# Performance work log

Measured on AMD Instinct MI355X. Metric: run time of the kernel, lower is better.

The kernel has to match this reference:

```python
import jax, jax.numpy as jnp
import numpy as np

D_MODEL = 1024
D_STATE = 128
HEAD_DIM = 64
EXPAND = 2
K = 4  # conv_kernel
N_GROUPS = 1
D_INNER = EXPAND * D_MODEL            # 2048
N_HEADS = D_INNER // HEAD_DIM         # 32
D_PROJ = 2 * D_INNER + 2 * N_GROUPS * D_STATE + N_HEADS  # 4384
EPS = 1e-6


def _rmsnorm(x, w):
    return x * jax.lax.rsqrt(jnp.mean(x * x, axis=-1, keepdims=True) + EPS) * w


def setup_inputs() -> dict:
    key = jax.random.key(0)
    ks = jax.random.split(key, 8)
    B, L = 2, 2048
    x = jax.random.normal(ks[0], (B, L, D_MODEL), jnp.float32)
    norm_w = jnp.ones((D_MODEL,), jnp.float32)
    in_proj_w = jax.random.normal(ks[1], (D_PROJ, D_MODEL), jnp.float32) / np.sqrt(D_MODEL).astype(np.float32)
    conv_w = jax.random.normal(ks[2], (D_INNER, K), jnp.float32) / np.sqrt(K).astype(np.float32)
    conv_b = jnp.zeros((D_INNER,), jnp.float32)
    A_log = jnp.log(jax.random.uniform(ks[3], (N_HEADS,), jnp.float32) * 15.0 + 1.0)
    D = jnp.ones((N_HEADS,), jnp.float32)
    dt_bias = jnp.log(jax.random.uniform(ks[4], (N_HEADS,), jnp.float32) * 0.099 + 0.001)
    out_proj_w = jax.random.normal(ks[5], (D_MODEL, D_INNER), jnp.float32) / np.sqrt(D_INNER).astype(np.float32)
    return dict(x=x, norm_w=norm_w, in_proj_w=in_proj_w, conv_w=conv_w, conv_b=conv_b,
                A_log=A_log, D=D, dt_bias=dt_bias, out_proj_w=out_proj_w)


def reference(x, norm_w, in_proj_w, conv_w, conv_b, A_log, D, dt_bias, out_proj_w):
    batch, L, _ = x.shape
    residual = x
    xn = _rmsnorm(x, norm_w)
    proj = jnp.einsum('bld,pd->blp', xn, in_proj_w)  # (B,L,D_PROJ)

    # split fused projection -> z, x_ssm, B, C, dt_raw
    i = 0
    z = proj[:, :, i:i + D_INNER]; i += D_INNER
    x_ssm = proj[:, :, i:i + D_INNER]; i += D_INNER
    bc = N_GROUPS * D_STATE
    Bm = proj[:, :, i:i + bc].reshape(batch, L, N_GROUPS, D_STATE); i += bc
    Cm = proj[:, :, i:i + bc].reshape(batch, L, N_GROUPS, D_STATE); i += bc
    dt_raw = proj[:, :, i:i + N_HEADS]

    # causal depthwise conv1d (left-pad K-1) + SiLU
    xp = jnp.pad(x_ssm, ((0, 0), (K - 1, 0), (0, 0)))
    x_conv = conv_b
    for k in range(K):
        x_conv = x_conv + xp[:, k:k + L, :] * conv_w[:, k]
    x_conv = jax.nn.silu(x_conv)

    xh = x_conv.reshape(batch, L, N_HEADS, HEAD_DIM)
    dt = jax.nn.softplus(dt_raw + dt_bias)          # (B,L,H)
    dA = jnp.exp(-jnp.exp(A_log) * dt)              # (B,L,H)
    dtx = dt[..., None] * xh                        # (B,L,H,P)

    gidx = jnp.arange(N_HEADS) // (N_HEADS // N_GROUPS)
    Bg = Bm[:, :, gidx, :]                          # (B,L,H,N)
    Cg = Cm[:, :, gidx, :]                          # (B,L,H,N)

    def step(h, inp):
        dA_t, dtx_t, B_t, C_t = inp                 # (B,H), (B,H,P), (B,H,N), (B,H,N)
        h = h * dA_t[:, :, None, None] + dtx_t[..., None] * B_t[:, :, None, :]
        y_t = jnp.einsum('bhpn,bhn->bhp', h, C_t)
        return h, y_t

    h0 = jnp.zeros((batch, N_HEADS, HEAD_DIM, D_STATE), jnp.float32)
    xs = (jnp.swapaxes(dA, 0, 1), jnp.swapaxes(dtx, 0, 1),
          jnp.swapaxes(Bg, 0, 1), jnp.swapaxes(Cg, 0, 1))
    _, ys = jax.lax.scan(step, h0, xs)              # ys: (L,B,H,P)
    y = jnp.swapaxes(ys, 0, 1) + D[None, None, :, None] * xh

    y = y.reshape(batch, L, D_INNER) * jax.nn.silu(z)
    return residual + jnp.einsum('bli,di->bld', y, out_proj_w)
```

## Files before the change

### kernel.cpp

```cpp
#include <hip/hip_runtime.h>
#include <hip/hip_bf16.h>

#define L_SEQ 2048
#define DM 1024
#define DI 2048
#define DS 128
#define NH 32
#define HD 64
#define DPROJ 4384
#define DPAD 4480
#define NBATCH 2
#define NCH 8
#define CH 256
#define B_OFF 4096
#define C_OFF 4224
#define DT_OFF 4352
#define SWZ(row) ((((row) ^ ((row) >> 3)) & 7) << 4)

typedef unsigned short u16;
typedef __attribute__((ext_vector_type(8))) short short8;
typedef __attribute__((ext_vector_type(4))) float f32x4;

#define GLL16(g, l)                                                     \
  __builtin_amdgcn_global_load_lds(                                     \
      (const __attribute__((address_space(1))) unsigned int*)(g),       \
      (__attribute__((address_space(3))) unsigned int*)(l), 16, 0, 0)
#define VMCNT0 asm volatile("s_waitcnt vmcnt(0)" ::: "memory")
#define SBAR __builtin_amdgcn_s_barrier()
#define SGB0 __builtin_amdgcn_sched_barrier(0)

__device__ __forceinline__ u16 f2bf(float f) {
  union { float f; unsigned u; } c; c.f = f;
  unsigned u = c.u;
  u += 0x7fffu + ((u >> 16) & 1u);
  return (u16)(u >> 16);
}
__device__ __forceinline__ float bf2f(u16 u) {
  return __uint_as_float((unsigned)u << 16);
}
__device__ __forceinline__ float siluf(float x) {
  return x / (1.0f + expf(-x));
}
__device__ __forceinline__ void store_out(u16* C, size_t o, float v) { C[o] = f2bf(v); }
__device__ __forceinline__ void store_out(float* C, size_t o, float v) { C[o] = v; }

__global__ __launch_bounds__(256) void rmsnorm_kernel(
    const float* __restrict__ x, const float* __restrict__ w,
    u16* __restrict__ xnb) {
  int m = blockIdx.x;
  int t = threadIdx.x;
  const float* row = x + (size_t)m * DM;
  float4 v = *(const float4*)(row + t * 4);
  float ss = v.x * v.x + v.y * v.y + v.z * v.z + v.w * v.w;
#pragma unroll
  for (int o = 32; o > 0; o >>= 1) ss += __shfl_xor(ss, o);
  __shared__ float sred[4];
  if ((t & 63) == 0) sred[t >> 6] = ss;
  __syncthreads();
  ss = sred[0] + sred[1] + sred[2] + sred[3];
  float rs = rsqrtf(ss * (1.0f / DM) + 1e-6f);
  float4 wv = *(const float4*)(w + t * 4);
  ushort4 o;
  o.x = f2bf(v.x * rs * wv.x);
  o.y = f2bf(v.y * rs * wv.y);
  o.z = f2bf(v.z * rs * wv.z);
  o.w = f2bf(v.w * rs * wv.w);
  *(ushort4*)(xnb + (size_t)m * DM + t * 4) = o;
}

__global__ __launch_bounds__(256) void cvt_w1_kernel(
    const float* __restrict__ w, u16* __restrict__ o) {
  int r = blockIdx.x;
  int c = threadIdx.x * 4;
  ushort4 u;
  if (r < DPROJ) {
    float4 v = *(const float4*)(w + (size_t)r * DM + c);
    u.x = f2bf(v.x); u.y = f2bf(v.y); u.z = f2bf(v.z); u.w = f2bf(v.w);
  } else {
    u.x = 0; u.y = 0; u.z = 0; u.w = 0;
  }
  *(ushort4*)(o + (size_t)r * DM + c) = u;
}

__global__ __launch_bounds__(256) void cvt_w2_kernel(
    const float* __restrict__ w, u16* __restrict__ o) {
  size_t i = ((size_t)blockIdx.x * 256 + threadIdx.x) * 8;
  float4 v0 = *(const float4*)(w + i);
  float4 v1 = *(const float4*)(w + i + 4);
  ushort4 a, b;
  a.x = f2bf(v0.x); a.y = f2bf(v0.y); a.z = f2bf(v0.z); a.w = f2bf(v0.w);
  b.x = f2bf(v1.x); b.y = f2bf(v1.y); b.z = f2bf(v1.z); b.w = f2bf(v1.w);
  *(ushort4*)(o + i) = a;
  *(ushort4*)(o + i + 4) = b;
}

template <typename OT, bool RES, bool DTS, int BN>
__global__ __launch_bounds__(256, 4) void gemm_bt(
    const u16* __restrict__ A, const u16* __restrict__ Bw,
    OT* __restrict__ C, const float* __restrict__ resid,
    float* __restrict__ dts, int M, int N, int K, int nbx) {
  constexpr int WN = BN / 2;
  constexpr int NJ = WN / 16;
  __shared__ u16 lA[2][128 * 32];
  __shared__ u16 lB[2][BN * 32];
  const int tid = threadIdx.x;
  const int wv = tid >> 6, lane = tid & 63;
  const int wm = wv >> 1, wn = wv & 1;

  const int nwg = gridDim.x;
  const int cpx = nwg >> 3;
  const int wg = blockIdx.x;
  const int swz = (wg & 7) * cpx + (wg >> 3);
  const int m0 = (swz / nbx) * 128, n0 = (swz % nbx) * BN;

  const int rowS = tid >> 2;
  const int colS = (tid & 3) * 8;
  const u16* gA0 = A + (size_t)(m0 + rowS) * K + colS;
  const u16* gA1 = A + (size_t)(m0 + rowS + 64) * K + colS;
  const u16* gB0 = Bw + (size_t)(n0 + rowS) * K + colS;
  const u16* gB1 = Bw + (size_t)(n0 + ((BN == 128) ? rowS + 64 : rowS)) * K + colS;

  auto stage = [&](int kt, int buf) {
    const int ko = kt << 5;
    GLL16(gA0 + ko, &lA[buf][wv * 512]);
    GLL16(gA1 + ko, &lA[buf][2048 + wv * 512]);
    GLL16(gB0 + ko, &lB[buf][wv * 512]);
    if (BN == 128) GLL16(gB1 + ko, &lB[buf][2048 + wv * 512]);
  };

  f32x4 acc[4][NJ] = {};
  const int r = lane & 15;
  const int koff = (lane >> 4) * 8;

  auto compute = [&](int buf) {
    short8 af[4], bfr[NJ];
#pragma unroll
    for (int i = 0; i < 4; ++i)
      af[i] = *(const short8*)&lA[buf][(wm * 64 + i * 16 + r) * 32 + koff];
#pragma unroll
    for (int j = 0; j < NJ; ++j)
      bfr[j] = *(const short8*)&lB[buf][(wn * WN + j * 16 + r) * 32 + koff];
#pragma unroll
    for (int i = 0; i < 4; ++i)
#pragma unroll
      for (int j = 0; j < NJ; ++j)
        acc[i][j] = __builtin_amdgcn_mfma_f32_16x16x32_bf16(
            af[i], bfr[j], acc[i][j], 0, 0, 0);
  };

  const int nk = K >> 5;
  stage(0, 0);
  VMCNT0;
  SBAR;
  SGB0;
  for (int kt = 0; kt < nk; kt += 2) {
    stage(kt + 1, 1);
    compute(0);
    VMCNT0;
    SBAR;
    SGB0;
    if (kt + 2 < nk) stage(kt + 2, 0);
    compute(1);
    VMCNT0;
    SBAR;
    SGB0;
  }

  const int rbase = m0 + wm * 64 + (lane >> 4) * 4;
  const int cbase = n0 + wn * WN + (lane & 15);
#pragma unroll
  for (int i = 0; i < 4; ++i) {
#pragma unroll
    for (int j = 0; j < NJ; ++j) {
      int row0 = rbase + i * 16;
      int col = cbase + j * 16;
#pragma unroll
      for (int rr = 0; rr < 4; ++rr) {
        size_t o = (size_t)(row0 + rr) * N + col;
        float v = acc[i][j][rr];
        if (RES) v += resid[o];
        store_out(C, o, v);
        if (DTS) {
          if (col >= DT_OFF && col < DT_OFF + NH)
            dts[(size_t)(row0 + rr) * NH + (col - DT_OFF)] = v;
        }
      }
    }
  }
}

__global__ __launch_bounds__(256) void conv_kernel(
    const u16* __restrict__ proj, const float* __restrict__ cw,
    const float* __restrict__ cb, u16* __restrict__ xh) {
  int m = blockIdx.x;
  int l = m & (L_SEQ - 1);
  int c0 = threadIdx.x * 8;
  float4 wv[8];
#pragma unroll
  for (int j = 0; j < 8; ++j) wv[j] = *(const float4*)(cw + (size_t)(c0 + j) * 4);
  float acc[8];
#pragma unroll
  for (int j = 0; j < 8; ++j) acc[j] = cb[c0 + j];
#pragma unroll
  for (int k = 0; k < 4; ++k) {
    int lk = l + k - 3;
    if (lk >= 0) {
      short8 rv8 = *(const short8*)(proj + (size_t)(m + k - 3) * DPAD + DI + c0);
#pragma unroll
      for (int j = 0; j < 8; ++j) {
        float wk = (k == 0) ? wv[j].x : (k == 1) ? wv[j].y : (k == 2) ? wv[j].z : wv[j].w;
        acc[j] = fmaf(bf2f((u16)rv8[j]), wk, acc[j]);
      }
    }
  }
  short8 o;
#pragma unroll
  for (int j = 0; j < 8; ++j) o[j] = (short)f2bf(siluf(acc[j]));
  *(short8*)(xh + (size_t)m * DI + c0) = o;
}

__global__ __launch_bounds__(256) void dtda_kernel(
    const float* __restrict__ dts, const float* __restrict__ dt_bias,
    const float* __restrict__ A_log, float* __restrict__ dAdt) {
  int idx = blockIdx.x * 256 + threadIdx.x;
  int h = idx & 31;
  float raw = dts[idx] + dt_bias[h];
  float dt = fmaxf(raw, 0.0f) + log1pf(expf(-fabsf(raw)));
  float a = -expf(A_log[h]) * dt;
  float2 o; o.x = a; o.y = dt;
  *(float2*)(dAdt + (size_t)idx * 2) = o;
}


__global__ __launch_bounds__(512) void scan_state_mfma(
    const u16* __restrict__ proj, const float* __restrict__ dAdt,
    const u16* __restrict__ xhy, float* __restrict__ S,
    float* __restrict__ P) {
  __shared__ u16 sBT[128 * 64];
  __shared__ u16 sXT[64 * 64];
  __shared__ u16 sXW[64 * 64];
  __shared__ float sDt[64], sCum[64], sWs[64], sLam[64];

  const int bid = blockIdx.x;
  const int ch = bid & 7, hh = (bid >> 3) & 31, b = bid >> 8;
  const int tid = threadIdx.x;
  const int w = tid >> 6, l = tid & 63;
  const int tw = w >> 1, half = w & 1;
  const int klane = (l >> 4) * 16;
  const size_t mchunk = (size_t)(b * L_SEQ + ch * CH);

  f32x4 hAcc[4] = {};
  float ctot = 0.0f;

  auto STAGE = [&](int sc) {
    const size_t m0 = mchunk + (size_t)sc * 64;
    {
      const int tp = tid >> 4;
      const int n0 = (tid & 15) * 8;
      const u16* r0 = proj + (m0 + 2 * tp) * DPAD + B_OFF + n0;
      short8 lo8 = *(const short8*)r0;
      short8 hi8 = *(const short8*)(r0 + DPAD);
#pragma unroll
      for (int q = 0; q < 8; ++q) {
        int n = n0 + q;
        unsigned v = (unsigned)(u16)lo8[q] | ((unsigned)(u16)hi8[q] << 16);
        *(unsigned*)((char*)sBT + ((n * 128 + 4 * tp) ^ SWZ(n))) = v;
      }
    }
    {
      const int sx = tid >> 3;
      const int p0 = (tid & 7) * 8;
      short8 xv8 = *(const short8*)(xhy + (m0 + sx) * DI + hh * 64 + p0);
#pragma unroll
      for (int i = 0; i < 8; ++i) {
        int p = p0 + i;
        *(u16*)((char*)sXT + ((p * 128 + 2 * sx) ^ SWZ(p))) = (u16)xv8[i];
      }
    }
    if (tid < 64) {
      float2 ad = *(const float2*)(dAdt + (m0 + tid) * 64 + hh * 2);
      float a = ad.x, dtv = ad.y;
      sDt[tid] = dtv;
      float val = a;
#pragma unroll
      for (int o = 1; o < 64; o <<= 1) {
        float t2 = __shfl_up(val, o);
        if (tid >= o) val += t2;
      }
      sCum[tid] = val;
      float c63 = __shfl(val, 63);
      sWs[tid] = __expf(c63 - val) * dtv;
      sLam[tid] = __expf(val);
    }
  };

  STAGE(0);
  __syncthreads();

  for (int sc = 0; sc < 4; ++sc) {
    {
      int p = tid >> 3, sg = tid & 7;
      int byteX = (p * 128 + sg * 16) ^ SWZ(p);
      short8 xv = *(short8*)((char*)sXT + byteX);
      short8 outp;
#pragma unroll
      for (int j = 0; j < 8; ++j)
        outp[j] = (short)f2bf(bf2f((u16)xv[j]) * sWs[sg * 8 + j]);
      *(short8*)((char*)sXW + byteX) = outp;
    }
    __syncthreads();

    {
      float lam63 = sLam[63];
      ctot += sCum[63];
#pragma unroll
      for (int j = 0; j < 4; ++j) {
        hAcc[j][0] *= lam63; hAcc[j][1] *= lam63;
        hAcc[j][2] *= lam63; hAcc[j][3] *= lam63;
      }
      int prow = tw * 16 + (l & 15);
      short8 aXW[2];
#pragma unroll
      for (int kk = 0; kk < 2; ++kk)
        aXW[kk] = *(short8*)((char*)sXW + ((prow * 128 + kk * 64 + klane) ^ SWZ(prow)));
#pragma unroll
      for (int j = 0; j < 4; ++j) {
        int nrow = (half * 4 + j) * 16 + (l & 15);
#pragma unroll
        for (int kk = 0; kk < 2; ++kk) {
          short8 bBT = *(short8*)((char*)sBT + ((nrow * 128 + kk * 64 + klane) ^ SWZ(nrow)));
          hAcc[j] = __builtin_amdgcn_mfma_f32_16x16x32_bf16(aXW[kk], bBT, hAcc[j], 0, 0, 0);
        }
      }
    }
    __syncthreads();
    if (sc < 3) STAGE(sc + 1);
    __syncthreads();
  }

  float* Sb = S + (size_t)((b * 32 + hh) * NCH + ch) * 8192;
  const int p0 = tw * 16 + (l >> 4) * 4;
#pragma unroll
  for (int j = 0; j < 4; ++j) {
    int n = (half * 4 + j) * 16 + (l & 15);
#pragma unroll
    for (int r = 0; r < 4; ++r)
      Sb[(p0 + r) * 128 + n] = hAcc[j][r];
  }
  if (tid == 0) P[(b * 32 + hh) * NCH + ch] = __expf(ctot);
}

__global__ __launch_bounds__(256) void combine_kernel(
    float* __restrict__ S, const float* __restrict__ P) {
  int tid = blockIdx.x * 256 + threadIdx.x;
  int bh = tid >> 13, pn = tid & 8191;
  size_t base = (size_t)bh * NCH * 8192 + pn;
  float E = 0.0f;
#pragma unroll
  for (int c = 0; c < NCH; ++c) {
    size_t o = base + (size_t)c * 8192;
    float Sc = S[o];
    S[o] = E;
    E = fmaf(P[bh * NCH + c], E, Sc);
  }
}

__global__ __launch_bounds__(512) void scan_y_mfma(
    const u16* __restrict__ proj, const float* __restrict__ dAdt,
    const u16* __restrict__ xhy, const float* __restrict__ Dv,
    const float* __restrict__ S, u16* __restrict__ yb) {
  __shared__ u16 sC[64 * 128];
  __shared__ u16 sB[64 * 128];
  __shared__ u16 sHb[64 * 128];
  __shared__ u16 sBT[128 * 64];
  __shared__ u16 sXT[64 * 64];
  __shared__ u16 sXW[64 * 64];
  __shared__ u16 sW[64 * 64];
  __shared__ float sDt[64], sCum[64], sWs[64], sLam[64];

  const int bid = blockIdx.x;
  const int ch = bid & 7, hh = (bid >> 3) & 31, b = bid >> 8;
  const int tid = threadIdx.x;
  const int w = tid >> 6, l = tid & 63;
  const int tw = w >> 1, half = w & 1;
  const int klane = (l >> 4) * 16;
  const float Dh = Dv[hh];
  const size_t mchunk = (size_t)(b * L_SEQ + ch * CH);

  f32x4 hAcc[4];
  {
    const float* Sb = S + (size_t)((b * 32 + hh) * NCH + ch) * 8192;
    const int p0 = tw * 16 + (l >> 4) * 4;
#pragma unroll
    for (int j = 0; j < 4; ++j) {
      int n = (half * 4 + j) * 16 + (l & 15);
#pragma unroll
      for (int r = 0; r < 4; ++r)
        hAcc[j][r] = Sb[(p0 + r) * 128 + n];
    }
    int p = tid >> 3, sg = tid & 7;
#pragma unroll
    for (int i = 0; i < 4; ++i) {
      float4 v = *(const float4*)(Sb + p * 128 + sg * 16 + 4 * i);
      ushort4 u;
      u.x = f2bf(v.x); u.y = f2bf(v.y); u.z = f2bf(v.z); u.w = f2bf(v.w);
      *(ushort4*)((char*)sHb + ((p * 256 + (sg * 16 + 4 * i) * 2) ^ SWZ(p))) = u;
    }
  }

  auto STAGE = [&](int sc) {
    const size_t m0 = mchunk + (size_t)sc * 64;
    {
      const int tp = tid >> 4;
      const int n0 = (tid & 15) * 8;
      const u16* r0 = proj + (m0 + 2 * tp) * DPAD;
      short8 b0 = *(const short8*)(r0 + B_OFF + n0);
      short8 b1 = *(const short8*)(r0 + DPAD + B_OFF + n0);
      short8 c0v = *(const short8*)(r0 + C_OFF + n0);
      short8 c1v = *(const short8*)(r0 + DPAD + C_OFF + n0);
      *(short8*)((char*)sB + ((2 * tp * 256 + n0 * 2) ^ SWZ(2 * tp))) = b0;
      *(short8*)((char*)sB + (((2 * tp + 1) * 256 + n0 * 2) ^ SWZ(2 * tp + 1))) = b1;
      *(short8*)((char*)sC + ((2 * tp * 256 + n0 * 2) ^ SWZ(2 * tp))) = c0v;
      *(short8*)((char*)sC + (((2 * tp + 1) * 256 + n0 * 2) ^ SWZ(2 * tp + 1))) = c1v;
#pragma unroll
      for (int q = 0; q < 8; ++q) {
        int n = n0 + q;
        unsigned v = (unsigned)(u16)b0[q] | ((unsigned)(u16)b1[q] << 16);
        *(unsigned*)((char*)sBT + ((n * 128 + 4 * tp) ^ SWZ(n))) = v;
      }
    }
    {
      const int sx = tid >> 3;
      const int p0 = (tid & 7) * 8;
      short8 xv8 = *(const short8*)(xhy + (m0 + sx) * DI + hh * 64 + p0);
#pragma unroll
      for (int i = 0; i < 8; ++i) {
        int p = p0 + i;
        *(u16*)((char*)sXT + ((p * 128 + 2 * sx) ^ SWZ(p))) = (u16)xv8[i];
      }
    }
    if (tid < 64) {
      float2 ad = *(const float2*)(dAdt + (m0 + tid) * 64 + hh * 2);
      float a = ad.x, dtv = ad.y;
      sDt[tid] = dtv;
      float val = a;
#pragma unroll
      for (int o = 1; o < 64; o <<= 1) {
        float t2 = __shfl_up(val, o);
        if (tid >= o) val += t2;
      }
      sCum[tid] = val;
      float c63 = __shfl(val, 63);
      sWs[tid] = __expf(c63 - val) * dtv;
      sLam[tid] = __expf(val);
    }
  };

  STAGE(0);
  __syncthreads();

  for (int sc = 0; sc < 4; ++sc) {
    const size_t m0 = mchunk + (size_t)sc * 64;
    {
      int p = tid >> 3, sg = tid & 7;
      int byteX = (p * 128 + sg * 16) ^ SWZ(p);
      short8 xv = *(short8*)((char*)sXT + byteX);
      short8 outp;
#pragma unroll
      for (int j = 0; j < 8; ++j)
        outp[j] = (short)f2bf(bf2f((u16)xv[j]) * sWs[sg * 8 + j]);
      *(short8*)((char*)sXW + byteX) = outp;
    }
    __syncthreads();

    const int trow = tw * 16 + (l & 15);
    short8 aC[4];
#pragma unroll
    for (int kk = 0; kk < 4; ++kk)
      aC[kk] = *(short8*)((char*)sC + ((trow * 256 + kk * 64 + klane) ^ SWZ(trow)));

    {
      f32x4 g[2] = {};
#pragma unroll
      for (int sv2 = 0; sv2 < 2; ++sv2) {
        int srow = (half * 2 + sv2) * 16 + (l & 15);
#pragma unroll
        for (int kk = 0; kk < 4; ++kk) {
          short8 bB = *(short8*)((char*)sB + ((srow * 256 + kk * 64 + klane) ^ SWZ(srow)));
          g[sv2] = __builtin_amdgcn_mfma_f32_16x16x32_bf16(aC[kk], bB, g[sv2], 0, 0, 0);
        }
      }
#pragma unroll
      for (int sv2 = 0; sv2 < 2; ++sv2) {
        int s = (half * 2 + sv2) * 16 + (l & 15);
        float dts_ = sDt[s], cums = sCum[s];
#pragma unroll
        for (int r = 0; r < 4; ++r) {
          int t = tw * 16 + (l >> 4) * 4 + r;
          float v = (t >= s) ? g[sv2][r] * __expf(sCum[t] - cums) * dts_ : 0.0f;
          *(u16*)((char*)sW + ((t * 128 + 2 * s) ^ SWZ(t))) = f2bf(v);
        }
      }
    }
    __syncthreads();

    f32x4 y1[2] = {}, y2[2] = {};
    float lamv[4], lam63 = sLam[63];
#pragma unroll
    for (int r = 0; r < 4; ++r) lamv[r] = sLam[tw * 16 + (l >> 4) * 4 + r];
    {
      short8 aW[2];
#pragma unroll
      for (int kk = 0; kk < 2; ++kk)
        aW[kk] = *(short8*)((char*)sW + ((trow * 128 + kk * 64 + klane) ^ SWZ(trow)));
#pragma unroll
      for (int pv2 = 0; pv2 < 2; ++pv2) {
        int prow = (half * 2 + pv2) * 16 + (l & 15);
#pragma unroll
        for (int kk = 0; kk < 2; ++kk) {
          short8 bX = *(short8*)((char*)sXT + ((prow * 128 + kk * 64 + klane) ^ SWZ(prow)));
          y1[pv2] = __builtin_amdgcn_mfma_f32_16x16x32_bf16(aW[kk], bX, y1[pv2], 0, 0, 0);
        }
#pragma unroll
        for (int kk = 0; kk < 4; ++kk) {
          short8 bH = *(short8*)((char*)sHb + ((prow * 256 + kk * 64 + klane) ^ SWZ(prow)));
          y2[pv2] = __builtin_amdgcn_mfma_f32_16x16x32_bf16(aC[kk], bH, y2[pv2], 0, 0, 0);
        }
      }
#pragma unroll
      for (int j = 0; j < 4; ++j) {
        hAcc[j][0] *= lam63; hAcc[j][1] *= lam63;
        hAcc[j][2] *= lam63; hAcc[j][3] *= lam63;
      }
      short8 aXW[2];
#pragma unroll
      for (int kk = 0; kk < 2; ++kk)
        aXW[kk] = *(short8*)((char*)sXW + ((trow * 128 + kk * 64 + klane) ^ SWZ(trow)));
#pragma unroll
      for (int j = 0; j < 4; ++j) {
        int nrow = (half * 4 + j) * 16 + (l & 15);
#pragma unroll
        for (int kk = 0; kk < 2; ++kk) {
          short8 bBT = *(short8*)((char*)sBT + ((nrow * 128 + kk * 64 + klane) ^ SWZ(nrow)));
          hAcc[j] = __builtin_amdgcn_mfma_f32_16x16x32_bf16(aXW[kk], bBT, hAcc[j], 0, 0, 0);
        }
      }
    }
    __syncthreads();

    {
#pragma unroll
      for (int j = 0; j < 4; ++j) {
        int n = (half * 4 + j) * 16 + (l & 15);
#pragma unroll
        for (int r = 0; r < 4; ++r) {
          int p = tw * 16 + (l >> 4) * 4 + r;
          *(u16*)((char*)sHb + ((p * 256 + 2 * n) ^ SWZ(p))) = f2bf(hAcc[j][r]);
        }
      }
#pragma unroll
      for (int pv2 = 0; pv2 < 2; ++pv2) {
        int p = (half * 2 + pv2) * 16 + (l & 15);
#pragma unroll
        for (int r = 0; r < 4; ++r) {
          int t = tw * 16 + (l >> 4) * 4 + r;
          int col = hh * 64 + p;
          size_t gy = (m0 + t) * DI + col;
          float xv = bf2f(xhy[gy]);
          float yv = y1[pv2][r] + lamv[r] * y2[pv2][r] + Dh * xv;
          float zv = bf2f(proj[(m0 + t) * DPAD + col]);
          yb[gy] = f2bf(yv * siluf(zv));
        }
      }
      if (sc < 3) STAGE(sc + 1);
    }
    __syncthreads();
  }
}

extern "C" void kernel_launch(void* const* d_in, const int* in_sizes, int n_in,
                              void* d_out, int out_size, void* d_ws, size_t ws_size,
                              hipStream_t stream) {
  const float* x      = (const float*)d_in[0];
  const float* norm_w = (const float*)d_in[1];
  const float* w1     = (const float*)d_in[2];
  const float* cw     = (const float*)d_in[3];
  const float* cb     = (const float*)d_in[4];
  const float* A_log  = (const float*)d_in[5];
  const float* Dv     = (const float*)d_in[6];
  const float* dt_b   = (const float*)d_in[7];
  const float* w2     = (const float*)d_in[8];
  float* out = (float*)d_out;

  char* ws = (char*)d_ws;
  u16*   xnb  = (u16*)(ws);
  u16*   w1b  = (u16*)(ws + 8388608);
  u16*   w2b  = (u16*)(ws + 17563648);
  u16*   proj = (u16*)(ws + 21757952);
  float* dts  = (float*)(ws + 58458112);
  u16*   xhy  = (u16*)(ws + 58982400);
  float* dAdt = (float*)(ws + 75759616);
  u16*   yb   = (u16*)(ws + 76808192);
  float* S    = (float*)(ws + 93585408);
  float* P    = (float*)(ws + 110362624);

  const int M = NBATCH * L_SEQ;

  rmsnorm_kernel<<<M, 256, 0, stream>>>(x, norm_w, xnb);
  cvt_w1_kernel<<<DPAD, 256, 0, stream>>>(w1, w1b);
  cvt_w2_kernel<<<1024, 256, 0, stream>>>(w2, w2b);
  gemm_bt<u16, false, true, 128><<<(DPAD / 128) * (M / 128), 256, 0, stream>>>(
      xnb, w1b, proj, nullptr, dts, M, DPAD, DM, DPAD / 128);
  conv_kernel<<<M, 256, 0, stream>>>(proj, cw, cb, xhy);
  dtda_kernel<<<M * NH / 256, 256, 0, stream>>>(dts, dt_b, A_log, dAdt);
  scan_state_mfma<<<512, 512, 0, stream>>>(proj, dAdt, xhy, S, P);
  combine_kernel<<<2048, 256, 0, stream>>>(S, P);
  scan_y_mfma<<<512, 512, 0, stream>>>(proj, dAdt, xhy, Dv, S, yb);
  gemm_bt<float, true, false, 64><<<(DM / 64) * (M / 128), 256, 0, stream>>>(
      yb, w2b, out, x, nullptr, M, DM, DI, DM / 64);
}
```

Measured before the change: 210.1 us.

## Triple-buffer GEMM LDS staging with partial vmcnt waits

After: 209.9 us. Within noise of the previous version (-0.1%).

```diff
diff --git a/kernel.cpp b/kernel.cpp
--- a/kernel.cpp
+++ b/kernel.cpp
@@ -25,9 +25,8 @@
   __builtin_amdgcn_global_load_lds(                                     \
       (const __attribute__((address_space(1))) unsigned int*)(g),       \
       (__attribute__((address_space(3))) unsigned int*)(l), 16, 0, 0)
-#define VMCNT0 asm volatile("s_waitcnt vmcnt(0)" ::: "memory")
 #define SBAR __builtin_amdgcn_s_barrier()
-#define SGB0 __builtin_amdgcn_sched_barrier(0)
+#define MEMFENCE asm volatile("" ::: "memory")
 
 __device__ __forceinline__ u16 f2bf(float f) {
   union { float f; unsigned u; } c; c.f = f;
@@ -101,8 +100,8 @@
     float* __restrict__ dts, int M, int N, int K, int nbx) {
   constexpr int WN = BN / 2;
   constexpr int NJ = WN / 16;
-  __shared__ u16 lA[2][128 * 32];
-  __shared__ u16 lB[2][BN * 32];
+  __shared__ u16 lA[3][128 * 32];
+  __shared__ u16 lB[3][BN * 32];
   const int tid = threadIdx.x;
   const int wv = tid >> 6, lane = tid & 63;
   const int wm = wv >> 1, wn = wv & 1;
@@ -118,7 +117,7 @@
   const u16* gA0 = A + (size_t)(m0 + rowS) * K + colS;
   const u16* gA1 = A + (size_t)(m0 + rowS + 64) * K + colS;
   const u16* gB0 = Bw + (size_t)(n0 + rowS) * K + colS;
-  const u16* gB1 = Bw + (size_t)(n0 + ((BN == 128) ? rowS + 64 : rowS)) * K + colS;
+  const u16* gB1 = Bw + (size_t)(n0 + rowS + 64) * K + colS;
 
   auto stage = [&](int kt, int buf) {
     const int ko = kt << 5;
@@ -150,20 +149,23 @@
 
   const int nk = K >> 5;
   stage(0, 0);
-  VMCNT0;
-  SBAR;
-  SGB0;
-  for (int kt = 0; kt < nk; kt += 2) {
-    stage(kt + 1, 1);
-    compute(0);
-    VMCNT0;
+  stage(1, 1);
+  int cur = 0;
+  for (int kt = 0; kt < nk; ++kt) {
+    if (kt + 1 < nk) {
+      if (BN == 128) asm volatile("s_waitcnt vmcnt(4)" ::: "memory");
+      else           asm volatile("s_waitcnt vmcnt(3)" ::: "memory");
+    } else {
+      asm volatile("s_waitcnt vmcnt(0)" ::: "memory");
+    }
     SBAR;
-    SGB0;
-    if (kt + 2 < nk) stage(kt + 2, 0);
-    compute(1);
-    VMCNT0;
-    SBAR;
-    SGB0;
+    MEMFENCE;
+    if (kt + 2 < nk) {
+      int nb = cur + 2; if (nb >= 3) nb -= 3;
+      stage(kt + 2, nb);
+    }
+    compute(cur);
+    ++cur; if (cur == 3) cur = 0;
   }
 
   const int rbase = m0 + wm * 64 + (lane >> 4) * 4;
```
